# Kernel tuning notes

Measured on AMD Instinct MI355X. Metric: run time of the kernel, lower is better.

## Reference

```python
import jax, jax.numpy as jnp
import numpy as np

INF = 100000.0
B, W, T, U, S, N = 64, 16, 64, 128, 20, 8


def setup_inputs() -> dict:
    key = jax.random.key(0)
    ks = jax.random.split(key, 9)
    xavier = (2.0 / (U + U)) ** 0.5
    return {
        "slot_utt_h": jax.random.normal(ks[0], (B, W, T, U), jnp.float32),
        "slot_candidate_c": jax.random.normal(ks[1], (S, U), jnp.float32),
        "status_candidate_c": jax.random.normal(ks[2], (N, U), jnp.float32),
        "position_encoding": jax.random.normal(ks[3], (B, W, S, U), jnp.float32),
        "q_status": jax.random.normal(ks[4], (B, W, N, U), jnp.float32),
        "mask": jnp.zeros((B, W, S * N), jnp.float32),
        "weight": jax.random.normal(ks[5], (U, U), jnp.float32) * xavier,  # bilinear co-attention weight [U,U]
        "W1": jax.random.normal(ks[6], (2 * U, U), jnp.float32) * 0.05,
        "b1": jnp.zeros((U,), jnp.float32),
        "W2": jax.random.normal(ks[7], (U, U), jnp.float32) * 0.05,
        "b2": jnp.zeros((U,), jnp.float32),
        "W3": jax.random.normal(ks[8], (U, 1), jnp.float32) * 0.05,
        "b3": jnp.zeros((1,), jnp.float32),
    }


def _zero_mask(p):
    # original: -(p == 0).float() * INF, added before softmax
    return jnp.where(p == 0.0, -INF, 0.0)


def reference(slot_utt_h, slot_candidate_c, status_candidate_c, position_encoding,
              q_status, mask, weight, W1, b1, W2, b2, W3, b3):
    # ---- attention over utterance tokens ----
    # p[b,w,s,t] = <slot_candidate_c[s], slot_utt_h[b,w,t]>
    p = jnp.einsum('su,bwtu->bwst', slot_candidate_c, slot_utt_h)
    p = jax.nn.softmax(p + _zero_mask(p), axis=-1)
    q_slot = jnp.einsum('bwst,bwtu->bwsu', p, slot_utt_h) + position_encoding  # [B,W,S,U]

    # ---- bilinear co-attention: [B,W*S,U] @ weight @ [B,U,W*N] -> [B,W,S,W,N] ----
    co = jnp.einsum('bwsu,uv,bxnv->bwsxn', q_slot, weight, q_status)
    p2 = jax.nn.softmax(co + _zero_mask(co), axis=3)  # softmax over the second window axis x

    # weighted sum of statuses over window axis x
    q_status_slot = jnp.einsum('bwsxn,bxnu->bwsnu', p2, q_status)  # [B,W,S,N,U]

    q_slot_exp = jnp.broadcast_to(q_slot[:, :, :, None, :], (B, W, S, N, U))
    features = jnp.concatenate([q_slot_exp, q_status_slot], axis=-1)  # [B,W,S,N,2U]

    # ---- MLP (dropout in eval mode = identity) ----
    h = jax.nn.relu(features @ W1 + b1)
    h = jax.nn.relu(h @ W2 + b2)
    logits = h @ W3 + b3  # [B,W,S,N,1]

    logits = logits.reshape(B, W, S * N)
    slot_pred_logits = jnp.max(logits + mask, axis=1)  # masked max-pool over window
    slot_pred_labels = (slot_pred_logits > 0.0).astype(jnp.float32)
    return (slot_pred_labels, S * N, slot_pred_logits)
```

## Files before the change

kernel.cpp:

```cpp
#include <hip/hip_runtime.h>
#include <math.h>

#define INF_ 100000.0f
constexpr int B_ = 64, W_ = 16, T_ = 64, U_ = 128, S_ = 20, N_ = 8;

typedef unsigned short ushort_t;
typedef __attribute__((ext_vector_type(8))) short bf16x8;
typedef __attribute__((ext_vector_type(4))) float floatx4;

static __device__ __forceinline__ unsigned short f2bf(float x) {
    unsigned int u = __float_as_uint(x);
    return (unsigned short)((u + 0x7fff + ((u >> 16) & 1)) >> 16);
}
static __device__ __forceinline__ float bf2f(unsigned short s) {
    return __uint_as_float(((unsigned int)s) << 16);
}

__global__ __launch_bounds__(256) void k0_cast(
    const float* __restrict__ q_status, const float* __restrict__ weight,
    const float* __restrict__ W1, const float* __restrict__ W2,
    const float* __restrict__ c,
    ushort_t* __restrict__ qstat_bf, ushort_t* __restrict__ wcomb,
    ushort_t* __restrict__ w1botT, ushort_t* __restrict__ w2T,
    ushort_t* __restrict__ c_bf)
{
    int idx = blockIdx.x * 256 + threadIdx.x;
    if (idx < 1048576) { qstat_bf[idx] = f2bf(q_status[idx]); return; }
    idx -= 1048576;
    if (idx < 32768) {
        int j = idx >> 7, k = idx & 127;
        float v = (j < 128) ? weight[k * 128 + j] : W1[k * 128 + (j - 128)];
        wcomb[idx] = f2bf(v); return;
    }
    idx -= 32768;
    if (idx < 16384) {
        int j = idx >> 7, k = idx & 127;
        w1botT[idx] = f2bf(W1[(128 + k) * 128 + j]); return;
    }
    idx -= 16384;
    if (idx < 16384) {
        int j = idx >> 7, k = idx & 127;
        w2T[idx] = f2bf(W2[k * 128 + j]); return;
    }
    idx -= 16384;
    if (idx < 4096) {
        int s = idx >> 7;
        c_bf[idx] = (s < 20) ? f2bf(c[idx]) : (ushort_t)0;
        return;
    }
}

__global__ __launch_bounds__(256) void k1_attn(
    const float* __restrict__ h,
    const ushort_t* __restrict__ c_bf,
    const float* __restrict__ pos,
    ushort_t* __restrict__ q_slot_bf)
{
    __shared__ __align__(16) ushort_t sh_h[64 * 136];
    __shared__ __align__(16) ushort_t sh_hT[128 * 72];
    __shared__ __align__(16) float    sh_sc[32 * 68];
    __shared__ __align__(16) ushort_t sh_P[32 * 72];

    const int bw = blockIdx.x, tid = threadIdx.x;
    const float* hb = h + (size_t)bw * 8192;
    for (int i = tid; i < 8192; i += 256) {
        int t = i >> 7, u = i & 127;
        ushort_t v = f2bf(hb[i]);
        sh_h[t * 136 + u] = v;
        sh_hT[u * 72 + t] = v;
    }
    for (int i = tid; i < 32 * 72; i += 256) sh_P[i] = 0;
    __syncthreads();

    const int wave = tid >> 6, lane = tid & 63, m16 = lane & 15, q = lane >> 4;

#pragma unroll
    for (int ci = 0; ci < 2; ++ci) {
        int cmb = wave * 2 + ci;
        int mt = cmb >> 2, jt = cmb & 3;
        floatx4 acc = {0.f, 0.f, 0.f, 0.f};
#pragma unroll
        for (int kt = 0; kt < 4; ++kt) {
            bf16x8 a = *(const bf16x8*)&c_bf[(mt * 16 + m16) * 128 + kt * 32 + q * 8];
            bf16x8 b = *(const bf16x8*)&sh_h[(jt * 16 + m16) * 136 + kt * 32 + q * 8];
            acc = __builtin_amdgcn_mfma_f32_16x16x32_bf16(a, b, acc, 0, 0, 0);
        }
#pragma unroll
        for (int reg = 0; reg < 4; ++reg)
            sh_sc[(mt * 16 + q * 4 + reg) * 68 + jt * 16 + m16] = acc[reg];
    }
    __syncthreads();

    for (int s = wave; s < 20; s += 4) {
        float v = sh_sc[s * 68 + lane];
        if (v == 0.0f) v = -INF_;
        float m = v;
        for (int d = 32; d; d >>= 1) m = fmaxf(m, __shfl_xor(m, d));
        float e = expf(v - m);
        float sum = e;
        for (int d = 32; d; d >>= 1) sum += __shfl_xor(sum, d);
        sh_P[s * 72 + lane] = f2bf(e / sum);
    }
    __syncthreads();

    const size_t obase = (size_t)bw * 2560;
#pragma unroll
    for (int ci = 0; ci < 4; ++ci) {
        int cmb = wave * 4 + ci;
        int mt = cmb >> 3, jt = cmb & 7;
        floatx4 acc = {0.f, 0.f, 0.f, 0.f};
#pragma unroll
        for (int kt = 0; kt < 2; ++kt) {
            bf16x8 a = *(const bf16x8*)&sh_P[(mt * 16 + m16) * 72 + kt * 32 + q * 8];
            bf16x8 b = *(const bf16x8*)&sh_hT[(jt * 16 + m16) * 72 + kt * 32 + q * 8];
            acc = __builtin_amdgcn_mfma_f32_16x16x32_bf16(a, b, acc, 0, 0, 0);
        }
        int u = jt * 16 + m16;
#pragma unroll
        for (int reg = 0; reg < 4; ++reg) {
            int row = mt * 16 + q * 4 + reg;
            if (row < 20)
                q_slot_bf[obase + row * 128 + u] =
                    f2bf(acc[reg] + pos[obase + row * 128 + u]);
        }
    }
}

__global__ __launch_bounds__(512, 2) void k2ab(
    const ushort_t* __restrict__ qs_bf,
    const ushort_t* __restrict__ wcomb,
    const float* __restrict__ b1,
    const ushort_t* __restrict__ qstat_bf,
    const ushort_t* __restrict__ w1botT,
    ushort_t* __restrict__ qw_bf,
    float* __restrict__ A,
    ushort_t* __restrict__ qs1T_bf)
{
    __shared__ __align__(16) ushort_t sh_w[256 * 136];
    const int tid = threadIdx.x;
    const int wave = tid >> 6, lane = tid & 63, m16 = lane & 15, q = lane >> 4;

    if (blockIdx.x < 160) {
        for (int i = tid * 4; i < 32768; i += 2048) {
            int j = i >> 7, k = i & 127;
            *(ushort4*)&sh_w[j * 136 + k] = *(const ushort4*)&wcomb[i];
        }
        __syncthreads();

        const size_t row = (size_t)blockIdx.x * 128 + wave * 16 + m16;
        floatx4 acc[16];
#pragma unroll
        for (int jt = 0; jt < 16; ++jt) acc[jt] = (floatx4){0.f, 0.f, 0.f, 0.f};
#pragma unroll
        for (int kt = 0; kt < 4; ++kt) {
            bf16x8 a = *(const bf16x8*)&qs_bf[row * 128 + kt * 32 + q * 8];
#pragma unroll
            for (int jt = 0; jt < 16; ++jt) {
                bf16x8 b = *(const bf16x8*)&sh_w[(jt * 16 + m16) * 136 + kt * 32 + q * 8];
                acc[jt] = __builtin_amdgcn_mfma_f32_16x16x32_bf16(a, b, acc[jt], 0, 0, 0);
            }
        }
        const size_t orow0 = (size_t)blockIdx.x * 128 + wave * 16 + q * 4;
#pragma unroll
        for (int jt = 0; jt < 16; ++jt) {
            int col = jt * 16 + m16;
            if (col < 128) {
#pragma unroll
                for (int reg = 0; reg < 4; ++reg)
                    qw_bf[(orow0 + reg) * 128 + col] = f2bf(acc[jt][reg]);
            } else {
                float bv = b1[col - 128];
#pragma unroll
                for (int reg = 0; reg < 4; ++reg)
                    A[(orow0 + reg) * 128 + (col - 128)] = acc[jt][reg] + bv;
            }
        }
    } else {
        const int blk = blockIdx.x - 160;
        for (int i = tid * 4; i < 16384; i += 2048) {
            int j = i >> 7, k = i & 127;
            *(ushort4*)&sh_w[j * 136 + k] = *(const ushort4*)&w1botT[i];
        }
        __syncthreads();

        const size_t row = (size_t)blk * 128 + wave * 16 + m16;
        floatx4 acc[8];
#pragma unroll
        for (int jt = 0; jt < 8; ++jt) acc[jt] = (floatx4){0.f, 0.f, 0.f, 0.f};
#pragma unroll
        for (int kt = 0; kt < 4; ++kt) {
            bf16x8 a = *(const bf16x8*)&qstat_bf[row * 128 + kt * 32 + q * 8];
#pragma unroll
            for (int jt = 0; jt < 8; ++jt) {
                bf16x8 b = *(const bf16x8*)&sh_w[(jt * 16 + m16) * 136 + kt * 32 + q * 8];
                acc[jt] = __builtin_amdgcn_mfma_f32_16x16x32_bf16(a, b, acc[jt], 0, 0, 0);
            }
        }
        const size_t orow0 = (size_t)blk * 128 + wave * 16 + q * 4;
#pragma unroll
        for (int jt = 0; jt < 8; ++jt) {
            int col = jt * 16 + m16;
#pragma unroll
            for (int reg = 0; reg < 4; ++reg) {
                size_t grow = orow0 + reg;
                qs1T_bf[(grow >> 7) * 16384 + (size_t)col * 128 + (grow & 127)]
                    = f2bf(acc[jt][reg]);
            }
        }
    }
}

__global__ __launch_bounds__(256) void k3_co(
    const ushort_t* __restrict__ qw_bf,
    const ushort_t* __restrict__ qstat_bf,
    ushort_t* __restrict__ co_bf)
{
    __shared__ __align__(16) ushort_t sh_y[128 * 136];
    const int tid = threadIdx.x, rt = blockIdx.x, b = blockIdx.y;
    for (int i = tid * 4; i < 16384; i += 1024) {
        int j = i >> 7, k = i & 127;
        *(ushort4*)&sh_y[j * 136 + k] = *(const ushort4*)&qstat_bf[(size_t)b * 16384 + i];
    }
    __syncthreads();

    const int wave = tid >> 6, lane = tid & 63, m16 = lane & 15, q = lane >> 4;
    const size_t rbase = (size_t)b * 320 + rt * 64 + wave * 16;

    floatx4 acc[8];
#pragma unroll
    for (int jt = 0; jt < 8; ++jt) acc[jt] = (floatx4){0.f, 0.f, 0.f, 0.f};
#pragma unroll
    for (int kt = 0; kt < 4; ++kt) {
        bf16x8 a = *(const bf16x8*)&qw_bf[(rbase + m16) * 128 + kt * 32 + q * 8];
#pragma unroll
        for (int jt = 0; jt < 8; ++jt) {
            bf16x8 b2_ = *(const bf16x8*)&sh_y[(jt * 16 + m16) * 136 + kt * 32 + q * 8];
            acc[jt] = __builtin_amdgcn_mfma_f32_16x16x32_bf16(a, b2_, acc[jt], 0, 0, 0);
        }
    }
#pragma unroll
    for (int jt = 0; jt < 8; ++jt)
#pragma unroll
        for (int reg = 0; reg < 4; ++reg)
            co_bf[(rbase + q * 4 + reg) * 128 + jt * 16 + m16] = f2bf(acc[jt][reg]);
}

__global__ __launch_bounds__(640, 5) void k4_fused(
    const ushort_t* __restrict__ co_bf,
    const ushort_t* __restrict__ qs1T_bf,
    const float* __restrict__ A,
    const ushort_t* __restrict__ w2T,
    const float* __restrict__ b2,
    const float* __restrict__ W3,
    const float* __restrict__ b3,
    float* __restrict__ lg)
{
    __shared__ __align__(16) ushort_t sh_w2t[128 * 136];
    __shared__ __align__(16) ushort_t sh_u[160 * 136];

    const int bw = blockIdx.x, b = bw >> 4, tid = threadIdx.x;

    for (int i = tid * 4; i < 16384; i += 2560) {
        int r = i >> 7, k = i & 127;
        *(ushort4*)&sh_w2t[r * 136 + k] = *(const ushort4*)&w2T[i];
        *(ushort4*)&sh_u[r * 136 + k] =
            *(const ushort4*)&qs1T_bf[(size_t)b * 16384 + i];
    }

    {
        int sn = tid >> 2, xi = tid & 3;
        int s = sn >> 3, n = sn & 7;
        const ushort_t* crow = co_bf + ((size_t)bw * 20 + s) * 128;
        float v[4];
        float m = -INFINITY;
#pragma unroll
        for (int j = 0; j < 4; ++j) {
            float t = bf2f(crow[(xi + 4 * j) * 8 + n]);
            if (t == 0.0f) t = -INF_;
            v[j] = t;
            m = fmaxf(m, t);
        }
        m = fmaxf(m, __shfl_xor(m, 1));
        m = fmaxf(m, __shfl_xor(m, 2));
        float sum = 0.f;
#pragma unroll
        for (int j = 0; j < 4; ++j) { v[j] = expf(v[j] - m); sum += v[j]; }
        sum += __shfl_xor(sum, 1);
        sum += __shfl_xor(sum, 2);
        float r = 1.0f / sum;
#pragma unroll
        for (int j = 0; j < 4; ++j)
            sh_u[17408 + s * 132 + (xi + 4 * j) * 8 + n] = f2bf(v[j] * r);
    }
    __syncthreads();

    const int wave = tid >> 6, lane = tid & 63, m16 = lane & 15, q = lane >> 4;
    const int n = m16 & 7;
    const int sIdx = wave * 2 + (m16 >> 3);
    const int rowS = wave * 16 + m16;

    floatx4 gacc[8];
#pragma unroll
    for (int mt = 0; mt < 8; ++mt) gacc[mt] = (floatx4){0.f, 0.f, 0.f, 0.f};

#pragma unroll
    for (int kt = 0; kt < 4; ++kt) {
        short pv = (short)sh_u[17408 + sIdx * 132 + kt * 32 + q * 8 + n];
        bf16x8 pf = {0, 0, 0, 0, 0, 0, 0, 0};
        pf[0] = (n == 0) ? pv : (short)0;
        pf[1] = (n == 1) ? pv : (short)0;
        pf[2] = (n == 2) ? pv : (short)0;
        pf[3] = (n == 3) ? pv : (short)0;
        pf[4] = (n == 4) ? pv : (short)0;
        pf[5] = (n == 5) ? pv : (short)0;
        pf[6] = (n == 6) ? pv : (short)0;
        pf[7] = (n == 7) ? pv : (short)0;
#pragma unroll
        for (int mt = 0; mt < 8; ++mt) {
            bf16x8 af = *(const bf16x8*)&sh_u[(mt * 16 + m16) * 136 + kt * 32 + q * 8];
            gacc[mt] = __builtin_amdgcn_mfma_f32_16x16x32_bf16(af, pf, gacc[mt], 0, 0, 0);
        }
    }
    __syncthreads();

    {
        const float* Ab = A + ((size_t)bw * 20 + sIdx) * 128;
#pragma unroll
        for (int mt = 0; mt < 8; ++mt) {
            int u0 = mt * 16 + q * 4;
            float4 av = *(const float4*)&Ab[u0];
            ushort4 o;
            o.x = f2bf(fmaxf(gacc[mt][0] + av.x, 0.f));
            o.y = f2bf(fmaxf(gacc[mt][1] + av.y, 0.f));
            o.z = f2bf(fmaxf(gacc[mt][2] + av.z, 0.f));
            o.w = f2bf(fmaxf(gacc[mt][3] + av.w, 0.f));
            *(ushort4*)&sh_u[rowS * 136 + u0] = o;
        }
    }
    __syncthreads();

    floatx4 acc[8];
#pragma unroll
    for (int jt = 0; jt < 8; ++jt) acc[jt] = (floatx4){0.f, 0.f, 0.f, 0.f};

#pragma unroll
    for (int kt = 0; kt < 4; ++kt) {
        const int k0 = kt * 32 + q * 8;
        bf16x8 af = *(const bf16x8*)&sh_u[rowS * 136 + k0];
#pragma unroll
        for (int jt = 0; jt < 8; ++jt) {
            bf16x8 bfr = *(const bf16x8*)&sh_w2t[(jt * 16 + m16) * 136 + k0];
            acc[jt] = __builtin_amdgcn_mfma_f32_16x16x32_bf16(af, bfr, acc[jt], 0, 0, 0);
        }
    }

    float b2v[8], w3v[8];
#pragma unroll
    for (int jt = 0; jt < 8; ++jt) {
        b2v[jt] = b2[jt * 16 + m16];
        w3v[jt] = W3[jt * 16 + m16];
    }
    const float b3v = b3[0];

#pragma unroll
    for (int reg = 0; reg < 4; ++reg) {
        float p = 0.f;
#pragma unroll
        for (int jt = 0; jt < 8; ++jt)
            p += fmaxf(acc[jt][reg] + b2v[jt], 0.f) * w3v[jt];
        p += __shfl_xor(p, 1);
        p += __shfl_xor(p, 2);
        p += __shfl_xor(p, 4);
        p += __shfl_xor(p, 8);
        if (m16 == 0)
            lg[(size_t)bw * 160 + wave * 16 + q * 4 + reg] = p + b3v;
    }
}

__global__ __launch_bounds__(256) void k5_final(
    const float* __restrict__ lg,
    const float* __restrict__ mask,
    float* __restrict__ out)
{
    int idx = blockIdx.x * 256 + threadIdx.x;
    const int SN = S_ * N_;
    if (idx < B_ * SN) {
        int b = idx / SN, sn = idx % SN;
        float m = -INFINITY;
        for (int w = 0; w < W_; ++w) {
            float v = lg[((size_t)b * W_ + w) * SN + sn] + mask[((size_t)b * W_ + w) * SN + sn];
            m = fmaxf(m, v);
        }
        out[idx] = (m > 0.f) ? 1.f : 0.f;
        out[B_ * SN + 1 + idx] = m;
    }
    if (idx == 0) out[B_ * SN] = (float)SN;
}

extern "C" void kernel_launch(void* const* d_in, const int* in_sizes, int n_in,
                              void* d_out, int out_size, void* d_ws, size_t ws_size,
                              hipStream_t stream) {
    const float* slot_utt_h = (const float*)d_in[0];
    const float* slot_candidate_c = (const float*)d_in[1];
    const float* position_encoding = (const float*)d_in[3];
    const float* q_status = (const float*)d_in[4];
    const float* mask = (const float*)d_in[5];
    const float* weight = (const float*)d_in[6];
    const float* W1 = (const float*)d_in[7];
    const float* b1 = (const float*)d_in[8];
    const float* W2 = (const float*)d_in[9];
    const float* b2 = (const float*)d_in[10];
    const float* W3 = (const float*)d_in[11];
    const float* b3 = (const float*)d_in[12];
    float* out = (float*)d_out;

    float* f = (float*)d_ws;
    ushort_t* q_slot_bf = (ushort_t*)(f + 0);
    ushort_t* qw_bf     = (ushort_t*)(f + 1310720);
    float*    A         = f + 2621440;
    ushort_t* qs1T_bf   = (ushort_t*)(f + 5242880);
    ushort_t* co_bf     = (ushort_t*)(f + 5767168);
    float*    lg        = f + 8388608;
    ushort_t* qstat_bf  = (ushort_t*)(f + 8552448);
    ushort_t* wcomb     = (ushort_t*)(f + 9076736);
    ushort_t* w1botT    = (ushort_t*)(f + 9093120);
    ushort_t* w2T       = (ushort_t*)(f + 9101312);
    ushort_t* c_bf      = (ushort_t*)(f + 9109504);

    k0_cast<<<4368, 256, 0, stream>>>(q_status, weight, W1, W2,
                                      slot_candidate_c,
                                      qstat_bf, wcomb, w1botT, w2T, c_bf);
    k1_attn<<<1024, 256, 0, stream>>>(slot_utt_h, c_bf,
                                      position_encoding, q_slot_bf);
    k2ab<<<224, 512, 0, stream>>>(q_slot_bf, wcomb, b1, qstat_bf, w1botT,
                                  qw_bf, A, qs1T_bf);
    k3_co<<<dim3(5, 64), 256, 0, stream>>>(qw_bf, qstat_bf, co_bf);
    k4_fused<<<1024, 640, 0, stream>>>(co_bf, qs1T_bf, A, w2T, b2, W3, b3, lg);
    k5_final<<<(B_ * S_ * N_ + 255) / 256, 256, 0, stream>>>(lg, mask, out);
}
```

Before: 181.9 us.

## Reassociate bilinear co-attention: precompute q_status·weightᵀ per batch, fuse scores into MLP kernel

```diff
diff --git a/kernel.cpp b/kernel.cpp
--- a/kernel.cpp
+++ b/kernel.cpp
@@ -20,33 +20,91 @@
     const float* __restrict__ q_status, const float* __restrict__ weight,
     const float* __restrict__ W1, const float* __restrict__ W2,
     const float* __restrict__ c,
-    ushort_t* __restrict__ qstat_bf, ushort_t* __restrict__ wcomb,
+    ushort_t* __restrict__ qstat_bf, ushort_t* __restrict__ w1topT,
     ushort_t* __restrict__ w1botT, ushort_t* __restrict__ w2T,
-    ushort_t* __restrict__ c_bf)
+    ushort_t* __restrict__ c_bf, ushort_t* __restrict__ Gt_bf)
 {
-    int idx = blockIdx.x * 256 + threadIdx.x;
-    if (idx < 1048576) { qstat_bf[idx] = f2bf(q_status[idx]); return; }
-    idx -= 1048576;
-    if (idx < 32768) {
-        int j = idx >> 7, k = idx & 127;
-        float v = (j < 128) ? weight[k * 128 + j] : W1[k * 128 + (j - 128)];
-        wcomb[idx] = f2bf(v); return;
-    }
-    idx -= 32768;
-    if (idx < 16384) {
-        int j = idx >> 7, k = idx & 127;
-        w1botT[idx] = f2bf(W1[(128 + k) * 128 + j]); return;
-    }
-    idx -= 16384;
-    if (idx < 16384) {
-        int j = idx >> 7, k = idx & 127;
-        w2T[idx] = f2bf(W2[k * 128 + j]); return;
-    }
-    idx -= 16384;
-    if (idx < 4096) {
-        int s = idx >> 7;
-        c_bf[idx] = (s < 20) ? f2bf(c[idx]) : (ushort_t)0;
+    __shared__ __align__(16) ushort_t sw[128 * 136];
+    __shared__ __align__(16) ushort_t sq[128 * 136];
+
+    const int tid = threadIdx.x;
+
+    if (blockIdx.x < 1076) {
+        int g = blockIdx.x * 256 + tid;
+        if (g < 262144) {
+            int i = g * 4;
+            float4 v = *(const float4*)&q_status[i];
+            ushort4 o = {f2bf(v.x), f2bf(v.y), f2bf(v.z), f2bf(v.w)};
+            *(ushort4*)&qstat_bf[i] = o;
+            return;
+        }
+        g -= 262144;
+        if (g < 4096) {
+            int i = g * 4, j = i >> 7, k = i & 127;
+            ushort4 o = {f2bf(W1[k * 128 + j]), f2bf(W1[(k + 1) * 128 + j]),
+                         f2bf(W1[(k + 2) * 128 + j]), f2bf(W1[(k + 3) * 128 + j])};
+            *(ushort4*)&w1topT[i] = o;
+            return;
+        }
+        g -= 4096;
+        if (g < 4096) {
+            int i = g * 4, j = i >> 7, k = i & 127;
+            ushort4 o = {f2bf(W1[(128 + k) * 128 + j]), f2bf(W1[(129 + k) * 128 + j]),
+                         f2bf(W1[(130 + k) * 128 + j]), f2bf(W1[(131 + k) * 128 + j])};
+            *(ushort4*)&w1botT[i] = o;
+            return;
+        }
+        g -= 4096;
+        if (g < 4096) {
+            int i = g * 4, j = i >> 7, k = i & 127;
+            ushort4 o = {f2bf(W2[k * 128 + j]), f2bf(W2[(k + 1) * 128 + j]),
+                         f2bf(W2[(k + 2) * 128 + j]), f2bf(W2[(k + 3) * 128 + j])};
+            *(ushort4*)&w2T[i] = o;
+            return;
+        }
+        g -= 4096;
+        if (g < 1024) {
+            int i = g * 4, s = i >> 7;
+            ushort4 o = {0, 0, 0, 0};
+            if (s < 20) {
+                float4 v = *(const float4*)&c[i];
+                o = (ushort4){f2bf(v.x), f2bf(v.y), f2bf(v.z), f2bf(v.w)};
+            }
+            *(ushort4*)&c_bf[i] = o;
+            return;
+        }
         return;
+    }
+
+    const int b = blockIdx.x - 1076;
+    const float* qb = q_status + (size_t)b * 16384;
+    for (int i = tid * 4; i < 16384; i += 1024) {
+        int r = i >> 7, v = i & 127;
+        float4 wv = *(const float4*)&weight[i];
+        ushort4 ow = {f2bf(wv.x), f2bf(wv.y), f2bf(wv.z), f2bf(wv.w)};
+        *(ushort4*)&sw[r * 136 + v] = ow;
+        float4 qv = *(const float4*)&qb[i];
+        ushort4 oq = {f2bf(qv.x), f2bf(qv.y), f2bf(qv.z), f2bf(qv.w)};
+        *(ushort4*)&sq[r * 136 + v] = oq;
+    }
+    __syncthreads();
+
+    const int wave = tid >> 6, lane = tid & 63, m16 = lane & 15, q = lane >> 4;
+    ushort_t* Gb = Gt_bf + (size_t)b * 16384;
+#pragma unroll
+    for (int ci = 0; ci < 16; ++ci) {
+        int tile = wave * 16 + ci;
+        int mt = tile >> 3, jt = tile & 7;
+        floatx4 acc = {0.f, 0.f, 0.f, 0.f};
+#pragma unroll
+        for (int kt = 0; kt < 4; ++kt) {
+            bf16x8 a = *(const bf16x8*)&sq[(mt * 16 + m16) * 136 + kt * 32 + q * 8];
+            bf16x8 w = *(const bf16x8*)&sw[(jt * 16 + m16) * 136 + kt * 32 + q * 8];
+            acc = __builtin_amdgcn_mfma_f32_16x16x32_bf16(a, w, acc, 0, 0, 0);
+        }
+#pragma unroll
+        for (int reg = 0; reg < 4; ++reg)
+            Gb[(mt * 16 + q * 4 + reg) * 128 + jt * 16 + m16] = f2bf(acc[reg]);
     }
 }
 
@@ -128,52 +186,45 @@
 
 __global__ __launch_bounds__(512, 2) void k2ab(
     const ushort_t* __restrict__ qs_bf,
-    const ushort_t* __restrict__ wcomb,
+    const ushort_t* __restrict__ w1topT,
     const float* __restrict__ b1,
     const ushort_t* __restrict__ qstat_bf,
     const ushort_t* __restrict__ w1botT,
-    ushort_t* __restrict__ qw_bf,
     float* __restrict__ A,
     ushort_t* __restrict__ qs1T_bf)
 {
-    __shared__ __align__(16) ushort_t sh_w[256 * 136];
+    __shared__ __align__(16) ushort_t sh_w[128 * 136];
     const int tid = threadIdx.x;
     const int wave = tid >> 6, lane = tid & 63, m16 = lane & 15, q = lane >> 4;
 
     if (blockIdx.x < 160) {
-        for (int i = tid * 4; i < 32768; i += 2048) {
+        for (int i = tid * 4; i < 16384; i += 2048) {
             int j = i >> 7, k = i & 127;
-            *(ushort4*)&sh_w[j * 136 + k] = *(const ushort4*)&wcomb[i];
+            *(ushort4*)&sh_w[j * 136 + k] = *(const ushort4*)&w1topT[i];
         }
         __syncthreads();
 
         const size_t row = (size_t)blockIdx.x * 128 + wave * 16 + m16;
-        floatx4 acc[16];
-#pragma unroll
-        for (int jt = 0; jt < 16; ++jt) acc[jt] = (floatx4){0.f, 0.f, 0.f, 0.f};
+        floatx4 acc[8];
+#pragma unroll
+        for (int jt = 0; jt < 8; ++jt) acc[jt] = (floatx4){0.f, 0.f, 0.f, 0.f};
 #pragma unroll
         for (int kt = 0; kt < 4; ++kt) {
             bf16x8 a = *(const bf16x8*)&qs_bf[row * 128 + kt * 32 + q * 8];
 #pragma unroll
-            for (int jt = 0; jt < 16; ++jt) {
+            for (int jt = 0; jt < 8; ++jt) {
                 bf16x8 b = *(const bf16x8*)&sh_w[(jt * 16 + m16) * 136 + kt * 32 + q * 8];
                 acc[jt] = __builtin_amdgcn_mfma_f32_16x16x32_bf16(a, b, acc[jt], 0, 0, 0);
             }
         }
         const size_t orow0 = (size_t)blockIdx.x * 128 + wave * 16 + q * 4;
 #pragma unroll
-        for (int jt = 0; jt < 16; ++jt) {
+        for (int jt = 0; jt < 8; ++jt) {
             int col = jt * 16 + m16;
-            if (col < 128) {
-#pragma unroll
-                for (int reg = 0; reg < 4; ++reg)
-                    qw_bf[(orow0 + reg) * 128 + col] = f2bf(acc[jt][reg]);
-            } else {
-                float bv = b1[col - 128];
-#pragma unroll
-                for (int reg = 0; reg < 4; ++reg)
-                    A[(orow0 + reg) * 128 + (col - 128)] = acc[jt][reg] + bv;
-            }
+            float bv = b1[col];
+#pragma unroll
+            for (int reg = 0; reg < 4; ++reg)
+                A[(orow0 + reg) * 128 + col] = acc[jt][reg] + bv;
         }
     } else {
         const int blk = blockIdx.x - 160;
@@ -210,43 +261,9 @@
     }
 }
 
-__global__ __launch_bounds__(256) void k3_co(
-    const ushort_t* __restrict__ qw_bf,
-    const ushort_t* __restrict__ qstat_bf,
-    ushort_t* __restrict__ co_bf)
-{
-    __shared__ __align__(16) ushort_t sh_y[128 * 136];
-    const int tid = threadIdx.x, rt = blockIdx.x, b = blockIdx.y;
-    for (int i = tid * 4; i < 16384; i += 1024) {
-        int j = i >> 7, k = i & 127;
-        *(ushort4*)&sh_y[j * 136 + k] = *(const ushort4*)&qstat_bf[(size_t)b * 16384 + i];
-    }
-    __syncthreads();
-
-    const int wave = tid >> 6, lane = tid & 63, m16 = lane & 15, q = lane >> 4;
-    const size_t rbase = (size_t)b * 320 + rt * 64 + wave * 16;
-
-    floatx4 acc[8];
-#pragma unroll
-    for (int jt = 0; jt < 8; ++jt) acc[jt] = (floatx4){0.f, 0.f, 0.f, 0.f};
-#pragma unroll
-    for (int kt = 0; kt < 4; ++kt) {
-        bf16x8 a = *(const bf16x8*)&qw_bf[(rbase + m16) * 128 + kt * 32 + q * 8];
-#pragma unroll
-        for (int jt = 0; jt < 8; ++jt) {
-            bf16x8 b2_ = *(const bf16x8*)&sh_y[(jt * 16 + m16) * 136 + kt * 32 + q * 8];
-            acc[jt] = __builtin_amdgcn_mfma_f32_16x16x32_bf16(a, b2_, acc[jt], 0, 0, 0);
-        }
-    }
-#pragma unroll
-    for (int jt = 0; jt < 8; ++jt)
-#pragma unroll
-        for (int reg = 0; reg < 4; ++reg)
-            co_bf[(rbase + q * 4 + reg) * 128 + jt * 16 + m16] = f2bf(acc[jt][reg]);
-}
-
 __global__ __launch_bounds__(640, 5) void k4_fused(
-    const ushort_t* __restrict__ co_bf,
+    const ushort_t* __restrict__ q_slot_bf,
+    const ushort_t* __restrict__ Gt_bf,
     const ushort_t* __restrict__ qs1T_bf,
     const float* __restrict__ A,
     const ushort_t* __restrict__ w2T,
@@ -256,7 +273,7 @@
     float* __restrict__ lg)
 {
     __shared__ __align__(16) ushort_t sh_w2t[128 * 136];
-    __shared__ __align__(16) ushort_t sh_u[160 * 136];
+    __shared__ __align__(16) ushort_t sh_u[22688];
 
     const int bw = blockIdx.x, b = bw >> 4, tid = threadIdx.x;
 
@@ -264,13 +281,50 @@
         int r = i >> 7, k = i & 127;
         *(ushort4*)&sh_w2t[r * 136 + k] = *(const ushort4*)&w2T[i];
         *(ushort4*)&sh_u[r * 136 + k] =
-            *(const ushort4*)&qs1T_bf[(size_t)b * 16384 + i];
-    }
+            *(const ushort4*)&Gt_bf[(size_t)b * 16384 + i];
+    }
+    __syncthreads();
+
+    const int wave = tid >> 6, lane = tid & 63, m16 = lane & 15, q = lane >> 4;
+
+    if (wave < 8) {
+        const ushort_t* qsl = q_slot_bf + (size_t)bw * 2560;
+        const bf16x8 zz = {0, 0, 0, 0, 0, 0, 0, 0};
+#pragma unroll
+        for (int ci = 0; ci < 2; ++ci) {
+            int tile = wave * 2 + ci;
+            int mt = tile >> 3, jt = tile & 7;
+            int arow = mt * 16 + m16;
+            floatx4 acc = {0.f, 0.f, 0.f, 0.f};
+#pragma unroll
+            for (int kt = 0; kt < 4; ++kt) {
+                bf16x8 a = (arow < 20)
+                    ? *(const bf16x8*)&qsl[arow * 128 + kt * 32 + q * 8] : zz;
+                bf16x8 g = *(const bf16x8*)&sh_u[(jt * 16 + m16) * 136 + kt * 32 + q * 8];
+                acc = __builtin_amdgcn_mfma_f32_16x16x32_bf16(a, g, acc, 0, 0, 0);
+            }
+#pragma unroll
+            for (int reg = 0; reg < 4; ++reg) {
+                int row = mt * 16 + q * 4 + reg;
+                if (row < 20)
+                    sh_u[20048 + row * 132 + jt * 16 + m16] = f2bf(acc[reg]);
+            }
+        }
+    }
+    __syncthreads();
 
     {
+        ushort4 rq[7];
+#pragma unroll 7
+        for (int jj = 0; jj < 7; ++jj) {
+            int i = tid * 4 + jj * 2560;
+            if (i < 16384)
+                rq[jj] = *(const ushort4*)&qs1T_bf[(size_t)b * 16384 + i];
+        }
+
         int sn = tid >> 2, xi = tid & 3;
         int s = sn >> 3, n = sn & 7;
-        const ushort_t* crow = co_bf + ((size_t)bw * 20 + s) * 128;
+        const ushort_t* crow = &sh_u[20048 + s * 132];
         float v[4];
         float m = -INFINITY;
 #pragma unroll
@@ -291,10 +345,18 @@
 #pragma unroll
         for (int j = 0; j < 4; ++j)
             sh_u[17408 + s * 132 + (xi + 4 * j) * 8 + n] = f2bf(v[j] * r);
-    }
-    __syncthreads();
-
-    const int wave = tid >> 6, lane = tid & 63, m16 = lane & 15, q = lane >> 4;
+
+#pragma unroll 7
+        for (int jj = 0; jj < 7; ++jj) {
+            int i = tid * 4 + jj * 2560;
+            if (i < 16384) {
+                int r2 = i >> 7, k2 = i & 127;
+                *(ushort4*)&sh_u[r2 * 136 + k2] = rq[jj];
+            }
+        }
+    }
+    __syncthreads();
+
     const int n = m16 & 7;
     const int sIdx = wave * 2 + (m16 >> 3);
     const int rowS = wave * 16 + m16;
@@ -416,25 +478,24 @@
 
     float* f = (float*)d_ws;
     ushort_t* q_slot_bf = (ushort_t*)(f + 0);
-    ushort_t* qw_bf     = (ushort_t*)(f + 1310720);
-    float*    A         = f + 2621440;
-    ushort_t* qs1T_bf   = (ushort_t*)(f + 5242880);
-    ushort_t* co_bf     = (ushort_t*)(f + 5767168);
-    float*    lg        = f + 8388608;
-    ushort_t* qstat_bf  = (ushort_t*)(f + 8552448);
-    ushort_t* wcomb     = (ushort_t*)(f + 9076736);
-    ushort_t* w1botT    = (ushort_t*)(f + 9093120);
-    ushort_t* w2T       = (ushort_t*)(f + 9101312);
-    ushort_t* c_bf      = (ushort_t*)(f + 9109504);
-
-    k0_cast<<<4368, 256, 0, stream>>>(q_status, weight, W1, W2,
+    float*    A         = f + 1310720;
+    ushort_t* qs1T_bf   = (ushort_t*)(f + 3932160);
+    ushort_t* Gt_bf     = (ushort_t*)(f + 4456448);
+    ushort_t* qstat_bf  = (ushort_t*)(f + 4980736);
+    float*    lg        = f + 5505024;
+    ushort_t* w1topT    = (ushort_t*)(f + 5668864);
+    ushort_t* w1botT    = (ushort_t*)(f + 5677056);
+    ushort_t* w2T       = (ushort_t*)(f + 5685248);
+    ushort_t* c_bf      = (ushort_t*)(f + 5693440);
+
+    k0_cast<<<1140, 256, 0, stream>>>(q_status, weight, W1, W2,
                                       slot_candidate_c,
-                                      qstat_bf, wcomb, w1botT, w2T, c_bf);
+                                      qstat_bf, w1topT, w1botT, w2T, c_bf, Gt_bf);
     k1_attn<<<1024, 256, 0, stream>>>(slot_utt_h, c_bf,
                                       position_encoding, q_slot_bf);
-    k2ab<<<224, 512, 0, stream>>>(q_slot_bf, wcomb, b1, qstat_bf, w1botT,
-                                  qw_bf, A, qs1T_bf);
-    k3_co<<<dim3(5, 64), 256, 0, stream>>>(qw_bf, qstat_bf, co_bf);
-    k4_fused<<<1024, 640, 0, stream>>>(co_bf, qs1T_bf, A, w2T, b2, W3, b3, lg);
+    k2ab<<<224, 512, 0, stream>>>(q_slot_bf, w1topT, b1, qstat_bf, w1botT,
+                                  A, qs1T_bf);
+    k4_fused<<<1024, 640, 0, stream>>>(q_slot_bf, Gt_bf, qs1T_bf, A, w2T,
+                                       b2, W3, b3, lg);
     k5_final<<<(B_ * S_ * N_ + 255) / 256, 256, 0, stream>>>(lg, mask, out);
 }
```

Result: no change. 181.6 us (-0.2%).
